# Performance work log

Measured on AMD Instinct MI355X. Metric: run time of the kernel, lower is better.

The kernel has to match this reference:

```python
import jax, jax.numpy as jnp
import numpy as np

H = 1024      # hidden_size
I = 512       # moe_intermediate_size
E = 8         # n_routed_experts
K = 2         # num_experts_per_tok
SI = I * 2    # shared expert intermediate (n_shared_experts=2)
B, S = 2, 1024


def setup_inputs() -> dict:
    key = jax.random.key(0)
    ks = jax.random.split(key, 9)
    s = 0.02
    return {
        "x": jax.random.normal(ks[0], (B, S, H), jnp.float32),
        "gate_w": jax.random.normal(ks[1], (E, H), jnp.float32) * s,
        "lb_bias": jnp.zeros((E,), jnp.float32),
        "expert_gate_w": jax.random.normal(ks[2], (E, I, H), jnp.float32) * s,
        "expert_up_w": jax.random.normal(ks[3], (E, I, H), jnp.float32) * s,
        "expert_down_w": jax.random.normal(ks[4], (E, H, I), jnp.float32) * s,
        "shared_gate_w": jax.random.normal(ks[5], (SI, H), jnp.float32) * s,
        "shared_up_w": jax.random.normal(ks[6], (SI, H), jnp.float32) * s,
        "shared_down_w": jax.random.normal(ks[7], (H, SI), jnp.float32) * s,
    }


def _mlp(x, gw, uw, dw):
    # SwiGLU: down( silu(gate(x)) * up(x) )
    return (jax.nn.silu(x @ gw.T) * (x @ uw.T)) @ dw.T


def reference(x, gate_w, lb_bias, expert_gate_w, expert_up_w, expert_down_w,
              shared_gate_w, shared_up_w, shared_down_w):
    b, s, h = x.shape
    xf = x.reshape(-1, h)                                   # [T, H]
    # --- SimpleRouter (sigmoid scoring) ---
    logits = xf @ gate_w.T + lb_bias                        # [T, E]
    scores = jax.nn.sigmoid(logits.astype(jnp.float32))
    topw, topi = jax.lax.top_k(scores, K)                   # [T, K]
    topw = (topw / (topw.sum(-1, keepdims=True) + 1e-8)).astype(x.dtype)
    # --- _process_local: per-expert dispatch/compute/combine ---
    # Faithful to torch source: expert_weights[mask].mean(dim=-1) collapses to a
    # SCALAR per expert (mean routing weight over all tokens sent to that expert).
    out = jnp.zeros_like(xf)
    for e in range(E):
        m = (topi == e)                                     # [T, K]
        sel = m.any(axis=-1)                                # [T]
        cnt = m.sum()
        wmean = (topw * m).sum() / jnp.maximum(cnt, 1).astype(topw.dtype)
        y = _mlp(xf, expert_gate_w[e], expert_up_w[e], expert_down_w[e])  # [T, H]
        out = out + jnp.where(sel[:, None], y * wmean, jnp.zeros((), x.dtype))
    out = out.reshape(b, s, h)
    # --- shared experts ---
    out = out + _mlp(x, shared_gate_w, shared_up_w, shared_down_w)
    return out
```

## Files before the change

### kernel.cpp

```cpp
#include <hip/hip_runtime.h>

#define H_DIM 1024
#define I_DIM 512
#define NE 8
#define SI_DIM 1024
#define NT 2048

typedef __bf16 bf16;
typedef __bf16 bf16x4 __attribute__((ext_vector_type(4)));
typedef __bf16 bf16x8 __attribute__((ext_vector_type(8)));
typedef float f32x4 __attribute__((ext_vector_type(4)));

#define W_GU 0ull
#define W_DN 8388608ull
#define W_SGU 12582912ull
#define W_SDN 14680064ull
#define W_TOT 15728640ull

#define NWB 15360
#define NRB 512

#define OFF_CNT 0
#define OFF_WM 64
#define OFF_TOPI 1024
#define OFF_TOPW (OFF_TOPI + NT * 8)
#define OFF_LISTS (OFF_TOPW + NT * 8)
#define OFF_WB (OFF_LISTS + NE * NT * 4)
#define OFF_XB (OFF_WB + (size_t)W_TOT * 2)
#define OFF_ACTE (OFF_XB + (size_t)NT * H_DIM * 2)
#define OFF_ACTS (OFF_ACTE + (size_t)NE * NT * I_DIM * 2)

__device__ __forceinline__ bf16x4 cvt4(f32x4 v) {
  bf16x4 r;
  r.x = (bf16)v.x; r.y = (bf16)v.y; r.z = (bf16)v.z; r.w = (bf16)v.w;
  return r;
}

__device__ __forceinline__ void glds16(const bf16* g, bf16* l) {
  __builtin_amdgcn_global_load_lds(
      (const __attribute__((address_space(1))) unsigned int*)g,
      (__attribute__((address_space(3))) unsigned int*)l, 16, 0, 0);
}

__global__ __launch_bounds__(256) void prep_kernel(
    const float* __restrict__ x, const float* __restrict__ gw,
    const float* __restrict__ lb, const float* __restrict__ eg,
    const float* __restrict__ eu, const float* __restrict__ ed,
    const float* __restrict__ sg, const float* __restrict__ su,
    const float* __restrict__ sd, bf16* __restrict__ wb,
    bf16* __restrict__ xb, int2* __restrict__ topi,
    float2* __restrict__ topw) {
  const int bx = blockIdx.x;
  const int tid = threadIdx.x;
  if (bx < NWB) {
    size_t i = ((size_t)bx * 256 + tid) * 4;
    const float* src;
    if (i < W_DN) {
      size_t z = i >> 20;
      int rem = (int)(i & ((1u << 20) - 1));
      int rp = rem >> 10, k = rem & 1023;
      int b = rp >> 4;
      int sr = ((b >> 1) << 4) | (rp & 15);
      src = ((b & 1) ? eu : eg) + (z << 19) + ((size_t)sr << 10) + k;
    } else if (i < W_SGU) {
      src = ed + (i - W_DN);
    } else if (i < W_SDN) {
      int rem = (int)(i - W_SGU);
      int rp = rem >> 10, k = rem & 1023;
      int b = rp >> 4;
      int sr = ((b >> 1) << 4) | (rp & 15);
      src = ((b & 1) ? su : sg) + ((size_t)sr << 10) + k;
    } else {
      src = sd + (i - W_SDN);
    }
    *(bf16x4*)(wb + i) = cvt4(*(const f32x4*)src);
  } else {
    const int lane = tid & 63;
    const int t = (bx - NWB) * 4 + (tid >> 6);
    const float* xr = x + (size_t)t * H_DIM;
    bf16* xw = xb + (size_t)t * H_DIM;
    float s[NE];
#pragma unroll
    for (int e = 0; e < NE; e++) s[e] = 0.f;
#pragma unroll
    for (int k0 = 0; k0 < H_DIM; k0 += 256) {
      f32x4 xv = *(const f32x4*)(xr + k0 + lane * 4);
      *(bf16x4*)(xw + k0 + lane * 4) = cvt4(xv);
#pragma unroll
      for (int e = 0; e < NE; e++) {
        f32x4 gv = *(const f32x4*)(gw + e * H_DIM + k0 + lane * 4);
        s[e] += xv.x * gv.x + xv.y * gv.y + xv.z * gv.z + xv.w * gv.w;
      }
    }
#pragma unroll
    for (int e = 0; e < NE; e++) {
      float v = s[e];
#pragma unroll
      for (int off = 32; off > 0; off >>= 1) v += __shfl_xor(v, off);
      s[e] = v;
    }
    if (lane == 0) {
      float sc[NE];
#pragma unroll
      for (int e = 0; e < NE; e++) sc[e] = 1.f / (1.f + expf(-(s[e] + lb[e])));
      int i1 = 0;
#pragma unroll
      for (int e = 1; e < NE; e++)
        if (sc[e] > sc[i1]) i1 = e;
      int i2 = -1;
#pragma unroll
      for (int e = 0; e < NE; e++) {
        if (e == i1) continue;
        if (i2 < 0 || sc[e] > sc[i2]) i2 = e;
      }
      float w1 = sc[i1], w2 = sc[i2];
      float inv = 1.f / (w1 + w2 + 1e-8f);
      topi[t] = make_int2(i1, i2);
      topw[t] = make_float2(w1 * inv, w2 * inv);
    }
  }
}

__global__ __launch_bounds__(256) void build_kernel(
    const int2* __restrict__ topi, const float2* __restrict__ topw,
    int* __restrict__ cnt, float* __restrict__ wm, int* __restrict__ lists) {
  const int e = blockIdx.x;
  const int wave = threadIdx.x >> 6, lane = threadIdx.x & 63;
  __shared__ int wc[4];
  __shared__ float wf[4];
  const int tbeg = wave * (NT / 4), tend = tbeg + NT / 4;

  int c = 0;
  float wa = 0.f;
  for (int t0 = tbeg; t0 < tend; t0 += 64) {
    int2 ti = topi[t0 + lane];
    float2 tw = topw[t0 + lane];
    bool hit = (ti.x == e) || (ti.y == e);
    float w = (ti.x == e) ? tw.x : ((ti.y == e) ? tw.y : 0.f);
    c += __popcll(__ballot(hit));
#pragma unroll
    for (int off = 32; off > 0; off >>= 1) w += __shfl_xor(w, off);
    wa += w;
  }
  if (lane == 0) { wc[wave] = c; wf[wave] = wa; }
  __syncthreads();
  int pos = 0;
  for (int w = 0; w < wave; w++) pos += wc[w];
  for (int t0 = tbeg; t0 < tend; t0 += 64) {
    int t = t0 + lane;
    int2 ti = topi[t];
    bool hit = (ti.x == e) || (ti.y == e);
    unsigned long long m = __ballot(hit);
    int pre = __popcll(m & ((1ull << lane) - 1ull));
    if (hit) lists[e * NT + pos + pre] = t;
    pos += __popcll(m);
  }
  if (threadIdx.x == 0) {
    int ctot = wc[0] + wc[1] + wc[2] + wc[3];
    cnt[e] = ctot;
    wm[e] = (wf[0] + wf[1] + wf[2] + wf[3]) / (float)(ctot > 0 ? ctot : 1);
  }
}

__global__ __launch_bounds__(256) void gemm_gu(
    const bf16* __restrict__ wb, const bf16* __restrict__ xb,
    const int* __restrict__ cnt, const int* __restrict__ lists,
    bf16* __restrict__ act_e, bf16* __restrict__ act_s) {
  const int b = blockIdx.x;
  int z, ct, rt;
  if (b < 1024) {
    z = b & 7;
    int q = b >> 3;
    ct = q & 7;
    rt = q >> 3;
  } else {
    z = NE;
    int s = b - 1024;
    ct = s & 15;
    rt = s >> 4;
  }
  const int tid = threadIdx.x;
  __shared__ int rows_s[128];
  __shared__ __align__(16) bf16 As[128 * 64];
  __shared__ __align__(16) bf16 Bs[128 * 64];
  int mrem, ldc;
  bf16* Cb;
  const bf16* Bb;
  if (z < NE) {
    int c = cnt[z];
    if (rt * 128 >= c) return;
    mrem = c - rt * 128;
    if (tid < 128)
      rows_s[tid] = lists[z * NT + rt * 128 + (tid < mrem ? tid : mrem - 1)];
    Bb = wb + W_GU + ((size_t)z << 20) + (size_t)ct * 128 * H_DIM;
    Cb = act_e + ((size_t)z * NT + rt * 128) * I_DIM;
    ldc = I_DIM;
  } else {
    mrem = 128;
    if (tid < 128) rows_s[tid] = rt * 128 + tid;
    Bb = wb + W_SGU + (size_t)ct * 128 * H_DIM;
    Cb = act_s + (size_t)rt * 128 * SI_DIM;
    ldc = SI_DIM;
  }
  __syncthreads();

  const int lane = tid & 63, wave = tid >> 6;
  const int mw = (wave & 1) * 64, nw = (wave >> 1) * 64;
  const int l15 = lane & 15, quad = lane >> 4;
  const int srow = tid >> 3;
  const int cch = tid & 7;
  const int p8 = cch * 8;
  const int sx = (l15 & 7) * 8;

  const bf16 *ap[4], *bp[4];
  int alo[4], blo[4];
#pragma unroll
  for (int r = 0; r < 4; r++) {
    int R = srow + r * 32;
    int gs = (cch ^ (R & 7)) * 8;
    ap[r] = xb + (size_t)rows_s[R] * H_DIM + gs;
    alo[r] = R * 64 + p8;
    bp[r] = Bb + (size_t)R * H_DIM + gs;
    blo[r] = R * 64 + p8;
  }

  f32x4 acc[4][4] = {};
  for (int k0 = 0; k0 < H_DIM; k0 += 64) {
#pragma unroll
    for (int r = 0; r < 4; r++) glds16(ap[r] + k0, &As[alo[r]]);
#pragma unroll
    for (int r = 0; r < 4; r++) glds16(bp[r] + k0, &Bs[blo[r]]);
    __syncthreads();
#pragma unroll
    for (int kk = 0; kk < 2; kk++) {
      const int ko = (kk * 4 + quad) * 8;
      bf16x8 av[4], bv[4];
#pragma unroll
      for (int i = 0; i < 4; i++)
        av[i] = *(const bf16x8*)&As[(mw + i * 16 + l15) * 64 + (ko ^ sx)];
#pragma unroll
      for (int j = 0; j < 4; j++)
        bv[j] = *(const bf16x8*)&Bs[(nw + j * 16 + l15) * 64 + (ko ^ sx)];
#pragma unroll
      for (int i = 0; i < 4; i++)
#pragma unroll
        for (int j = 0; j < 4; j++)
          acc[i][j] = __builtin_amdgcn_mfma_f32_16x16x32_bf16(av[i], bv[j], acc[i][j], 0, 0, 0);
    }
    __syncthreads();
  }

#pragma unroll
  for (int i = 0; i < 4; i++) {
#pragma unroll
    for (int rg = 0; rg < 4; rg++) {
      int rl = mw + i * 16 + quad * 4 + rg;
      if (rl < mrem) {
#pragma unroll
        for (int jp = 0; jp < 2; jp++) {
          float g = acc[i][jp * 2][rg];
          float u = acc[i][jp * 2 + 1][rg];
          int c = ct * 64 + (nw >> 1) + jp * 16 + l15;
          Cb[(size_t)rl * ldc + c] = (bf16)((g / (1.f + __expf(-g))) * u);
        }
      }
    }
  }
}

__global__ __launch_bounds__(256) void gemm_down(
    const bf16* __restrict__ wb, const bf16* __restrict__ act_e,
    const bf16* __restrict__ act_s, const int* __restrict__ cnt,
    const float* __restrict__ wm, const int* __restrict__ lists,
    float* __restrict__ out) {
  const int b = blockIdx.x;
  int z, ct, rt;
  if (b < 1024) {
    z = b & 7;
    int q = b >> 3;
    ct = q & 7;
    rt = q >> 3;
  } else {
    z = NE;
    int s = b - 1024;
    ct = s & 7;
    rt = s >> 3;
  }
  const int tid = threadIdx.x;
  __shared__ int rows_s[128];
  __shared__ __align__(16) bf16 As[128 * 64];
  __shared__ __align__(16) bf16 Bs[128 * 64];
  int K, mrem;
  const bf16 *Ab, *Bb;
  if (z < NE) {
    int c = cnt[z];
    if (rt * 128 >= c) return;
    mrem = c - rt * 128;
    if (tid < 128)
      rows_s[tid] = lists[z * NT + rt * 128 + (tid < mrem ? tid : mrem - 1)];
    Ab = act_e + ((size_t)z * NT + rt * 128) * I_DIM;
    K = I_DIM;
    Bb = wb + W_DN + ((size_t)z << 19) + (size_t)ct * 128 * I_DIM;
  } else {
    mrem = 128;
    if (tid < 128) rows_s[tid] = rt * 128 + tid;
    Ab = act_s + (size_t)rt * 128 * SI_DIM;
    K = SI_DIM;
    Bb = wb + W_SDN + (size_t)ct * 128 * SI_DIM;
  }
  __syncthreads();

  const int lane = tid & 63, wave = tid >> 6;
  const int mw = (wave & 1) * 64, nw = (wave >> 1) * 64;
  const int l15 = lane & 15, quad = lane >> 4;
  const int srow = tid >> 3;
  const int cch = tid & 7;
  const int p8 = cch * 8;
  const int sx = (l15 & 7) * 8;

  const bf16 *ap[4], *bp[4];
  int alo[4], blo[4];
#pragma unroll
  for (int r = 0; r < 4; r++) {
    int R = srow + r * 32;
    int gs = (cch ^ (R & 7)) * 8;
    ap[r] = Ab + (size_t)R * K + gs;
    alo[r] = R * 64 + p8;
    bp[r] = Bb + (size_t)R * K + gs;
    blo[r] = R * 64 + p8;
  }

  f32x4 acc[4][4] = {};
  for (int k0 = 0; k0 < K; k0 += 64) {
#pragma unroll
    for (int r = 0; r < 4; r++) glds16(ap[r] + k0, &As[alo[r]]);
#pragma unroll
    for (int r = 0; r < 4; r++) glds16(bp[r] + k0, &Bs[blo[r]]);
    __syncthreads();
#pragma unroll
    for (int kk = 0; kk < 2; kk++) {
      const int ko = (kk * 4 + quad) * 8;
      bf16x8 av[4], bv[4];
#pragma unroll
      for (int i = 0; i < 4; i++)
        av[i] = *(const bf16x8*)&As[(mw + i * 16 + l15) * 64 + (ko ^ sx)];
#pragma unroll
      for (int j = 0; j < 4; j++)
        bv[j] = *(const bf16x8*)&Bs[(nw + j * 16 + l15) * 64 + (ko ^ sx)];
#pragma unroll
      for (int i = 0; i < 4; i++)
#pragma unroll
        for (int j = 0; j < 4; j++)
          acc[i][j] = __builtin_amdgcn_mfma_f32_16x16x32_bf16(av[i], bv[j], acc[i][j], 0, 0, 0);
    }
    __syncthreads();
  }

  const float wsc = (z < NE) ? wm[z] : 1.f;
#pragma unroll
  for (int i = 0; i < 4; i++) {
#pragma unroll
    for (int rg = 0; rg < 4; rg++) {
      int rl = mw + i * 16 + quad * 4 + rg;
      if (rl < mrem) {
        int t = rows_s[rl];
        float* orow = out + (size_t)t * H_DIM + ct * 128 + nw;
#pragma unroll
        for (int j = 0; j < 4; j++)
          atomicAdd(&orow[j * 16 + l15], wsc * acc[i][j][rg]);
      }
    }
  }
}

extern "C" void kernel_launch(void* const* d_in, const int* in_sizes, int n_in,
                              void* d_out, int out_size, void* d_ws,
                              size_t ws_size, hipStream_t stream) {
  (void)in_sizes; (void)n_in; (void)out_size; (void)ws_size;
  const float* x  = (const float*)d_in[0];
  const float* gw = (const float*)d_in[1];
  const float* lb = (const float*)d_in[2];
  const float* eg = (const float*)d_in[3];
  const float* eu = (const float*)d_in[4];
  const float* ed = (const float*)d_in[5];
  const float* sg = (const float*)d_in[6];
  const float* su = (const float*)d_in[7];
  const float* sd = (const float*)d_in[8];
  float* out = (float*)d_out;
  char* ws = (char*)d_ws;

  int* cnt     = (int*)(ws + OFF_CNT);
  float* wm    = (float*)(ws + OFF_WM);
  int2* topi   = (int2*)(ws + OFF_TOPI);
  float2* topw = (float2*)(ws + OFF_TOPW);
  int* lists   = (int*)(ws + OFF_LISTS);
  bf16* wb     = (bf16*)(ws + OFF_WB);
  bf16* xb     = (bf16*)(ws + OFF_XB);
  bf16* act_e  = (bf16*)(ws + OFF_ACTE);
  bf16* act_s  = (bf16*)(ws + OFF_ACTS);

  hipMemsetAsync(d_out, 0, (size_t)NT * H_DIM * sizeof(float), stream);
  prep_kernel<<<NWB + NRB, 256, 0, stream>>>(x, gw, lb, eg, eu, ed, sg, su, sd,
                                             wb, xb, topi, topw);
  build_kernel<<<NE, 256, 0, stream>>>(topi, topw, cnt, wm, lists);
  gemm_gu<<<1280, 256, 0, stream>>>(wb, xb, cnt, lists, act_e, act_s);
  gemm_down<<<1152, 256, 0, stream>>>(wb, act_e, act_s, cnt, wm, lists, out);
}
```

Baseline: 210.5 us.

## Double-buffer LDS tiles in both GEMMs and fold output zeroing into prep

Both grouped GEMM kernels now use two LDS buffers, so the next K-slice is fetched with global_load_lds while the current slice feeds the MFMAs. This replaces the two block barriers per iteration with one waitcnt plus barrier. The shared row-index table is removed and each thread reads the routing list directly, which drops a barrier and adds some redundant global reads. The separate memset of the output is replaced by extra blocks in the prep kernel, saving a launch. LDS use per block doubles to 64KB, which may lower occupancy.

```diff
diff --git a/kernel.cpp b/kernel.cpp
--- a/kernel.cpp
+++ b/kernel.cpp
@@ -19,6 +19,7 @@
 
 #define NWB 15360
 #define NRB 512
+#define NZB 2048
 
 #define OFF_CNT 0
 #define OFF_WM 64
@@ -49,7 +50,7 @@
     const float* __restrict__ sg, const float* __restrict__ su,
     const float* __restrict__ sd, bf16* __restrict__ wb,
     bf16* __restrict__ xb, int2* __restrict__ topi,
-    float2* __restrict__ topw) {
+    float2* __restrict__ topw, float* __restrict__ out) {
   const int bx = blockIdx.x;
   const int tid = threadIdx.x;
   if (bx < NWB) {
@@ -74,7 +75,7 @@
       src = sd + (i - W_SDN);
     }
     *(bf16x4*)(wb + i) = cvt4(*(const f32x4*)src);
-  } else {
+  } else if (bx < NWB + NRB) {
     const int lane = tid & 63;
     const int t = (bx - NWB) * 4 + (tid >> 6);
     const float* xr = x + (size_t)t * H_DIM;
@@ -118,6 +119,10 @@
       topi[t] = make_int2(i1, i2);
       topw[t] = make_float2(w1 * inv, w2 * inv);
     }
+  } else {
+    size_t j = ((size_t)(bx - NWB - NRB) * 256 + tid) * 4;
+    f32x4 zz = {0.f, 0.f, 0.f, 0.f};
+    *(f32x4*)(out + j) = zz;
   }
 }
 
@@ -180,9 +185,8 @@
     rt = s >> 4;
   }
   const int tid = threadIdx.x;
-  __shared__ int rows_s[128];
-  __shared__ __align__(16) bf16 As[128 * 64];
-  __shared__ __align__(16) bf16 Bs[128 * 64];
+  __shared__ __align__(16) bf16 As[2 * 128 * 64];
+  __shared__ __align__(16) bf16 Bs[2 * 128 * 64];
   int mrem, ldc;
   bf16* Cb;
   const bf16* Bb;
@@ -190,19 +194,15 @@
     int c = cnt[z];
     if (rt * 128 >= c) return;
     mrem = c - rt * 128;
-    if (tid < 128)
-      rows_s[tid] = lists[z * NT + rt * 128 + (tid < mrem ? tid : mrem - 1)];
     Bb = wb + W_GU + ((size_t)z << 20) + (size_t)ct * 128 * H_DIM;
     Cb = act_e + ((size_t)z * NT + rt * 128) * I_DIM;
     ldc = I_DIM;
   } else {
     mrem = 128;
-    if (tid < 128) rows_s[tid] = rt * 128 + tid;
     Bb = wb + W_SGU + (size_t)ct * 128 * H_DIM;
     Cb = act_s + (size_t)rt * 128 * SI_DIM;
     ldc = SI_DIM;
   }
-  __syncthreads();
 
   const int lane = tid & 63, wave = tid >> 6;
   const int mw = (wave & 1) * 64, nw = (wave >> 1) * 64;
@@ -218,36 +218,50 @@
   for (int r = 0; r < 4; r++) {
     int R = srow + r * 32;
     int gs = (cch ^ (R & 7)) * 8;
-    ap[r] = xb + (size_t)rows_s[R] * H_DIM + gs;
+    int Rc = (z < NE) ? lists[z * NT + rt * 128 + (R < mrem ? R : mrem - 1)]
+                      : rt * 128 + R;
+    ap[r] = xb + (size_t)Rc * H_DIM + gs;
     alo[r] = R * 64 + p8;
     bp[r] = Bb + (size_t)R * H_DIM + gs;
     blo[r] = R * 64 + p8;
   }
 
   f32x4 acc[4][4] = {};
+#pragma unroll
+  for (int r = 0; r < 4; r++) glds16(ap[r], &As[alo[r]]);
+#pragma unroll
+  for (int r = 0; r < 4; r++) glds16(bp[r], &Bs[blo[r]]);
+  asm volatile("s_waitcnt vmcnt(0)" ::: "memory");
+  __builtin_amdgcn_s_barrier();
+  int cur = 0;
   for (int k0 = 0; k0 < H_DIM; k0 += 64) {
-#pragma unroll
-    for (int r = 0; r < 4; r++) glds16(ap[r] + k0, &As[alo[r]]);
-#pragma unroll
-    for (int r = 0; r < 4; r++) glds16(bp[r] + k0, &Bs[blo[r]]);
-    __syncthreads();
+    if (k0 + 64 < H_DIM) {
+      const int nx = (cur ^ 1) * 8192;
+#pragma unroll
+      for (int r = 0; r < 4; r++) glds16(ap[r] + k0 + 64, &As[nx + alo[r]]);
+#pragma unroll
+      for (int r = 0; r < 4; r++) glds16(bp[r] + k0 + 64, &Bs[nx + blo[r]]);
+    }
+    const int cb = cur * 8192;
 #pragma unroll
     for (int kk = 0; kk < 2; kk++) {
       const int ko = (kk * 4 + quad) * 8;
       bf16x8 av[4], bv[4];
 #pragma unroll
       for (int i = 0; i < 4; i++)
-        av[i] = *(const bf16x8*)&As[(mw + i * 16 + l15) * 64 + (ko ^ sx)];
+        av[i] = *(const bf16x8*)&As[cb + (mw + i * 16 + l15) * 64 + (ko ^ sx)];
 #pragma unroll
       for (int j = 0; j < 4; j++)
-        bv[j] = *(const bf16x8*)&Bs[(nw + j * 16 + l15) * 64 + (ko ^ sx)];
+        bv[j] = *(const bf16x8*)&Bs[cb + (nw + j * 16 + l15) * 64 + (ko ^ sx)];
 #pragma unroll
       for (int i = 0; i < 4; i++)
 #pragma unroll
         for (int j = 0; j < 4; j++)
           acc[i][j] = __builtin_amdgcn_mfma_f32_16x16x32_bf16(av[i], bv[j], acc[i][j], 0, 0, 0);
     }
-    __syncthreads();
+    asm volatile("s_waitcnt vmcnt(0)" ::: "memory");
+    __builtin_amdgcn_s_barrier();
+    cur ^= 1;
   }
 
 #pragma unroll
@@ -287,28 +301,23 @@
     rt = s >> 3;
   }
   const int tid = threadIdx.x;
-  __shared__ int rows_s[128];
-  __shared__ __align__(16) bf16 As[128 * 64];
-  __shared__ __align__(16) bf16 Bs[128 * 64];
+  __shared__ __align__(16) bf16 As[2 * 128 * 64];
+  __shared__ __align__(16) bf16 Bs[2 * 128 * 64];
   int K, mrem;
   const bf16 *Ab, *Bb;
   if (z < NE) {
     int c = cnt[z];
     if (rt * 128 >= c) return;
     mrem = c - rt * 128;
-    if (tid < 128)
-      rows_s[tid] = lists[z * NT + rt * 128 + (tid < mrem ? tid : mrem - 1)];
     Ab = act_e + ((size_t)z * NT + rt * 128) * I_DIM;
     K = I_DIM;
     Bb = wb + W_DN + ((size_t)z << 19) + (size_t)ct * 128 * I_DIM;
   } else {
     mrem = 128;
-    if (tid < 128) rows_s[tid] = rt * 128 + tid;
     Ab = act_s + (size_t)rt * 128 * SI_DIM;
     K = SI_DIM;
     Bb = wb + W_SDN + (size_t)ct * 128 * SI_DIM;
   }
-  __syncthreads();
 
   const int lane = tid & 63, wave = tid >> 6;
   const int mw = (wave & 1) * 64, nw = (wave >> 1) * 64;
@@ -331,29 +340,41 @@
   }
 
   f32x4 acc[4][4] = {};
+#pragma unroll
+  for (int r = 0; r < 4; r++) glds16(ap[r], &As[alo[r]]);
+#pragma unroll
+  for (int r = 0; r < 4; r++) glds16(bp[r], &Bs[blo[r]]);
+  asm volatile("s_waitcnt vmcnt(0)" ::: "memory");
+  __builtin_amdgcn_s_barrier();
+  int cur = 0;
   for (int k0 = 0; k0 < K; k0 += 64) {
-#pragma unroll
-    for (int r = 0; r < 4; r++) glds16(ap[r] + k0, &As[alo[r]]);
-#pragma unroll
-    for (int r = 0; r < 4; r++) glds16(bp[r] + k0, &Bs[blo[r]]);
-    __syncthreads();
+    if (k0 + 64 < K) {
+      const int nx = (cur ^ 1) * 8192;
+#pragma unroll
+      for (int r = 0; r < 4; r++) glds16(ap[r] + k0 + 64, &As[nx + alo[r]]);
+#pragma unroll
+      for (int r = 0; r < 4; r++) glds16(bp[r] + k0 + 64, &Bs[nx + blo[r]]);
+    }
+    const int cb = cur * 8192;
 #pragma unroll
     for (int kk = 0; kk < 2; kk++) {
       const int ko = (kk * 4 + quad) * 8;
       bf16x8 av[4], bv[4];
 #pragma unroll
       for (int i = 0; i < 4; i++)
-        av[i] = *(const bf16x8*)&As[(mw + i * 16 + l15) * 64 + (ko ^ sx)];
+        av[i] = *(const bf16x8*)&As[cb + (mw + i * 16 + l15) * 64 + (ko ^ sx)];
 #pragma unroll
       for (int j = 0; j < 4; j++)
-        bv[j] = *(const bf16x8*)&Bs[(nw + j * 16 + l15) * 64 + (ko ^ sx)];
+        bv[j] = *(const bf16x8*)&Bs[cb + (nw + j * 16 + l15) * 64 + (ko ^ sx)];
 #pragma unroll
       for (int i = 0; i < 4; i++)
 #pragma unroll
         for (int j = 0; j < 4; j++)
           acc[i][j] = __builtin_amdgcn_mfma_f32_16x16x32_bf16(av[i], bv[j], acc[i][j], 0, 0, 0);
     }
-    __syncthreads();
+    asm volatile("s_waitcnt vmcnt(0)" ::: "memory");
+    __builtin_amdgcn_s_barrier();
+    cur ^= 1;
   }
 
   const float wsc = (z < NE) ? wm[z] : 1.f;
@@ -363,7 +384,7 @@
     for (int rg = 0; rg < 4; rg++) {
       int rl = mw + i * 16 + quad * 4 + rg;
       if (rl < mrem) {
-        int t = rows_s[rl];
+        int t = (z < NE) ? lists[z * NT + rt * 128 + rl] : rt * 128 + rl;
         float* orow = out + (size_t)t * H_DIM + ct * 128 + nw;
 #pragma unroll
         for (int j = 0; j < 4; j++)
@@ -399,9 +420,9 @@
   bf16* act_e  = (bf16*)(ws + OFF_ACTE);
   bf16* act_s  = (bf16*)(ws + OFF_ACTS);
 
-  hipMemsetAsync(d_out, 0, (size_t)NT * H_DIM * sizeof(float), stream);
-  prep_kernel<<<NWB + NRB, 256, 0, stream>>>(x, gw, lb, eg, eu, ed, sg, su, sd,
-                                             wb, xb, topi, topw);
+  prep_kernel<<<NWB + NRB + NZB, 256, 0, stream>>>(x, gw, lb, eg, eu, ed, sg,
+                                                   su, sd, wb, xb, topi, topw,
+                                                   out);
   build_kernel<<<NE, 256, 0, stream>>>(topi, topw, cnt, wm, lists);
   gemm_gu<<<1280, 256, 0, stream>>>(wb, xb, cnt, lists, act_e, act_s);
   gemm_down<<<1152, 256, 0, stream>>>(wb, act_e, act_s, cnt, wm, lists, out);
```

Result: faster. 201.5 us (-4.3%).
